# Performance work log

Hardware: AMD Instinct MI355X
Metric: run time of the kernel (lower is better)

Reference implementation:

```python
import jax, jax.numpy as jnp
import numpy as np

C = 1024
T = 2048
B = 8

def setup_inputs() -> dict:
    key = jax.random.key(0)
    ks = jax.random.split(key, 7)
    s = lambda fan_in: 1.0 / np.sqrt(fan_in)
    return {
        "x":     jax.random.normal(ks[0], (B, T, C), dtype=jnp.float32),
        "w_qkv": jax.random.uniform(ks[1], (C, 3 * C), jnp.float32, -s(C), s(C)),
        "w_proj": jax.random.uniform(ks[2], (C, C), jnp.float32, -s(C), s(C)),
        "w1":    jax.random.uniform(ks[3], (C, 2 * C), jnp.float32, -s(C), s(C)),
        "w2":    jax.random.uniform(ks[4], (2 * C, C), jnp.float32, -s(2 * C), s(2 * C)),
        "g1":    jnp.ones((C,), jnp.float32),
        "g2":    jnp.ones((C,), jnp.float32),
    }

def rmsnorm(x, g, eps=1e-6):
    return x * jax.lax.rsqrt(jnp.mean(x * x, axis=-1, keepdims=True) + eps) * g

def reference(x, w_qkv, w_proj, w1, w2, g1, g2):
    t = x.shape[1]
    # --- attention ---
    h = rmsnorm(x, g1)
    qkv = h @ w_qkv                               # [B,T,3C]
    q, k, v = jnp.split(qkv, 3, axis=-1)
    scores = jnp.einsum('bqc,bkc->bqk', q, k) * (C ** -0.5)  # [B,T,T]
    causal = jnp.triu(jnp.ones((t, t), dtype=bool), k=1)
    scores = jnp.where(causal, -jnp.inf, scores)
    attn = jax.nn.softmax(scores, axis=-1)
    x = x + (attn @ v) @ w_proj
    # --- ffn ---
    h = rmsnorm(x, g2)
    return x + (jax.nn.silu(h @ w1)) @ w2
```

## Files before the change

### kernel.cpp

```cpp
#include <hip/hip_runtime.h>
#include <hip/hip_bf16.h>
#include <stdint.h>


#define C_DIM 1024
#define T_DIM 2048
#define B_DIM 8

typedef float f32x4 __attribute__((ext_vector_type(4)));
typedef __bf16 bf16x8 __attribute__((ext_vector_type(8)));

typedef const __attribute__((address_space(1))) void gvoid_t;
typedef __attribute__((address_space(3))) void lvoid_t;

__device__ __forceinline__ void gload_lds16(const void* g, void* l) {
    __builtin_amdgcn_global_load_lds((gvoid_t*)g, (lvoid_t*)l, 16, 0, 0);
}

__device__ __forceinline__ unsigned short f2bf_bits(float f) {
    __hip_bfloat16 h = __float2bfloat16(f);
    return *reinterpret_cast<unsigned short*>(&h);
}

__device__ __forceinline__ void xcd_remap(int& bx, int& by, int& bz) {
    const int gx = gridDim.x, gy = gridDim.y;
    const int nwg = gx * gy * (int)gridDim.z;
    const int orig = bx + gx * (by + gy * bz);
    const int q = nwg >> 3, r = nwg & 7;
    const int xcd = orig & 7, pos = orig >> 3;
    const int neu = (xcd < r ? xcd * (q + 1) : r * (q + 1) + (xcd - r) * q) + pos;
    bx = neu % gx;
    const int t = neu / gx;
    by = t % gy;
    bz = t / gy;
}

#define RD_A(dst, buf, hq) do { \
    _Pragma("unroll") \
    for (int mf_ = 0; mf_ < 4; ++mf_) { \
        const char* p_ = lds + (buf)*32768 + wrb + (hq)*8192 + mf_*2048; \
        dst[mf_][0] = *(const bf16x8*)(p_ + offk0); \
        dst[mf_][1] = *(const bf16x8*)(p_ + offk1); \
    } \
} while(0)

#define RD_B(dst, buf, nh) do { \
    _Pragma("unroll") \
    for (int n2_ = 0; n2_ < 2; ++n2_) { \
        const char* p_ = lds + 65536 + (buf)*32768 + wcb + ((nh)*2 + n2_)*2048; \
        dst[n2_][0] = *(const bf16x8*)(p_ + offk0); \
        dst[n2_][1] = *(const bf16x8*)(p_ + offk1); \
    } \
} while(0)

#define MMQ(aS, bS, Mh, Nh) do { \
    _Pragma("unroll") \
    for (int m4_ = 0; m4_ < 4; ++m4_) \
    _Pragma("unroll") \
    for (int n2_ = 0; n2_ < 2; ++n2_) \
    _Pragma("unroll") \
    for (int ks_ = 0; ks_ < 2; ++ks_) \
        acc[(Mh)*4 + m4_][(Nh)*2 + n2_] = __builtin_amdgcn_mfma_f32_16x16x32_bf16( \
            aS[m4_][ks_], bS[n2_][ks_], acc[(Mh)*4 + m4_][(Nh)*2 + n2_], 0, 0, 0); \
} while(0)

#define STA(buf, half, kt) do { \
    const int go_ = aoff + (half)*128*lda + (kt)*64; \
    char* lp_ = ldsw + (buf)*32768 + (half)*16384; \
    gload_lds16(A + go_,            lp_); \
    gload_lds16(A + go_ + 64*lda,   lp_ + 8192); \
} while(0)
#define STB(buf, half, kt) do { \
    const int go_ = boff + (half)*128*ldb + (kt)*64; \
    char* lp_ = ldsw + 65536 + (buf)*32768 + (half)*16384; \
    gload_lds16(Bt + go_,           lp_); \
    gload_lds16(Bt + go_ + 64*ldb,  lp_ + 8192); \
} while(0)

#define TILE_BODY(t, STG) do { \
    const int buf_ = (t) & 1; \
    bf16x8 a0[4][2], a1[4][2], b0v[2][2], b1v[2][2]; \
    RD_A(a0, buf_, 0); RD_A(a1, buf_, 1); \
    RD_B(b0v, buf_, 0); RD_B(b1v, buf_, 1); \
    __builtin_amdgcn_s_setprio(1); \
    MMQ(a0, b0v, 0, 0); MMQ(a0, b1v, 0, 1); \
    MMQ(a1, b0v, 1, 0); MMQ(a1, b1v, 1, 1); \
    __builtin_amdgcn_s_setprio(0); \
    asm volatile("s_waitcnt lgkmcnt(0)" ::: "memory"); \
    asm volatile("s_waitcnt vmcnt(0)" ::: "memory"); \
    __builtin_amdgcn_s_barrier(); \
    if (STG) { STB(buf_,0,(t)+2); STB(buf_,1,(t)+2); \
               STA(buf_,0,(t)+2); STA(buf_,1,(t)+2); } \
} while(0)

template<int EPI, int CMODE>
__global__ __launch_bounds__(512, 2)
void gemm256(const __hip_bfloat16* A, const __hip_bfloat16* Bt,
             void* Cout, const float* R, void* C2, void* C3,
             int K, int lda, int ldb, int ldc,
             long long sA, long long sB, long long sC, float scale)
{
    int bx = blockIdx.x, by = blockIdx.y, bz = blockIdx.z;
    xcd_remap(bx, by, bz);
    if constexpr (CMODE == 1) { if (bx > by) return; }

    const int tid  = threadIdx.x;
    const int lane = tid & 63, wave = tid >> 6;
    const int l15  = lane & 15, l4 = lane >> 4;
    const int wr   = wave >> 2, wc = wave & 3;
    const int m0   = by * 256, n0 = bx * 256;
    const int z    = bz;

    A  += (long long)z * sA;
    Bt += (long long)z * sB;

    __shared__ __align__(16) char lds_[131072];
    char* lds  = lds_;
    char* ldsw = lds_ + wave * 1024;

    int kmax = K;
    if constexpr (CMODE == 2) { int km = m0 + 256; kmax = km < K ? km : K; }
    const int NT = kmax >> 6;

    const int offk0 = l15 * 128 + (((l4)     ^ (l15 & 7)) << 4);
    const int offk1 = l15 * 128 + (((4 + l4) ^ (l15 & 7)) << 4);
    const int wrb = wr * 16384, wcb = wc * 8192;

    const int rowq  = tid >> 3;
    const int sslot = (tid & 7) ^ (rowq & 7);
    const int aoff  = (m0 + rowq) * lda + sslot * 8;
    const int boff  = (n0 + rowq) * ldb + sslot * 8;

    f32x4 acc[8][4];
#pragma unroll
    for (int i = 0; i < 8; ++i)
#pragma unroll
        for (int j = 0; j < 4; ++j) acc[i][j] = (f32x4){0.f, 0.f, 0.f, 0.f};

    STB(0, 0, 0); STB(0, 1, 0); STA(0, 0, 0); STA(0, 1, 0);
    STB(1, 0, 1); STB(1, 1, 1); STA(1, 0, 1); STA(1, 1, 1);
    asm volatile("s_waitcnt vmcnt(8)" ::: "memory");
    __builtin_amdgcn_s_barrier();

    int t = 0;
    for (; t < NT - 2; ++t) TILE_BODY(t, true);
    for (; t < NT; ++t)     TILE_BODY(t, false);

    asm volatile("s_waitcnt vmcnt(0)" ::: "memory");

    const long long cbase = (long long)z * sC;
#pragma unroll
    for (int mf = 0; mf < 8; ++mf) {
        const int rbase = m0 + wr * 128 + mf * 16 + l4 * 4;
#pragma unroll
        for (int nf = 0; nf < 4; ++nf) {
            const int col = n0 + wc * 64 + nf * 16 + l15;
#pragma unroll
            for (int r = 0; r < 4; ++r) {
                const float v = acc[mf][nf][r];
                const int row = rbase + r;
                if constexpr (EPI == 6) {
                    const int seg = col >> 10, ncol = col & 1023;
                    if (seg == 0) {
                        ((__hip_bfloat16*)Cout)[(long long)row * 1024 + ncol] =
                            __float2bfloat16(v);
                    } else if (seg == 1) {
                        ((__hip_bfloat16*)C2)[(long long)row * 1024 + ncol] =
                            __float2bfloat16(v);
                    } else {
                        const int b = row >> 11, tt = row & 2047;
                        ((__hip_bfloat16*)C3)[((long long)b * C_DIM + ncol) * T_DIM + tt] =
                            __float2bfloat16(v);
                    }
                } else {
                    const long long idx = cbase + (long long)row * ldc + col;
                    if constexpr (EPI == 0) {
                        ((__hip_bfloat16*)Cout)[idx] = __float2bfloat16(v);
                    } else if constexpr (EPI == 2) {
                        ((float*)Cout)[idx] = v + R[idx];
                    } else if constexpr (EPI == 3) {
                        const float s = v / (1.f + __expf(-v));
                        ((__hip_bfloat16*)Cout)[idx] = __float2bfloat16(s);
                    } else {
                        ((__hip_bfloat16*)Cout)[idx] = __float2bfloat16(v * scale);
                    }
                }
            }
        }
    }
}

__global__ __launch_bounds__(256)
void rmsnorm_kernel(const float* __restrict__ x, const float* __restrict__ g,
                    __hip_bfloat16* __restrict__ out)
{
    const long long row = blockIdx.x;
    const int tid = threadIdx.x;
    const float4 v = ((const float4*)(x + row * C_DIM))[tid];
    float ss = v.x * v.x + v.y * v.y + v.z * v.z + v.w * v.w;
#pragma unroll
    for (int off = 32; off; off >>= 1) ss += __shfl_xor(ss, off);
    __shared__ float red[4];
    if ((tid & 63) == 0) red[tid >> 6] = ss;
    __syncthreads();
    ss = red[0] + red[1] + red[2] + red[3];
    const float sc = rsqrtf(ss * (1.0f / C_DIM) + 1e-6f);
    const float4 gv = ((const float4*)g)[tid];
    ushort4 u;
    u.x = f2bf_bits(v.x * sc * gv.x);
    u.y = f2bf_bits(v.y * sc * gv.y);
    u.z = f2bf_bits(v.z * sc * gv.z);
    u.w = f2bf_bits(v.w * sc * gv.w);
    *(ushort4*)(out + row * C_DIM + tid * 4) = u;
}

__global__ __launch_bounds__(256)
void softmax_causal(__hip_bfloat16* __restrict__ SP)
{
    const int i = blockIdx.x, b = blockIdx.y;
    __hip_bfloat16* row = SP + ((long long)b * T_DIM + i) * T_DIM;
    const int tid = threadIdx.x;
    const int jbase = tid * 8;

    uint4 raw = ((const uint4*)row)[tid];
    float v[8];
    const unsigned w[4] = {raw.x, raw.y, raw.z, raw.w};
#pragma unroll
    for (int c = 0; c < 4; ++c) {
        unsigned lo = w[c] << 16;
        unsigned hi = w[c] & 0xFFFF0000u;
        v[2 * c]     = __uint_as_float(lo);
        v[2 * c + 1] = __uint_as_float(hi);
    }
#pragma unroll
    for (int e = 0; e < 8; ++e)
        if (jbase + e > i) v[e] = -1e30f;

    float m = v[0];
#pragma unroll
    for (int e = 1; e < 8; ++e) m = fmaxf(m, v[e]);
#pragma unroll
    for (int off = 32; off; off >>= 1) m = fmaxf(m, __shfl_xor(m, off));
    __shared__ float redm[4], reds[4];
    if ((tid & 63) == 0) redm[tid >> 6] = m;
    __syncthreads();
    m = fmaxf(fmaxf(redm[0], redm[1]), fmaxf(redm[2], redm[3]));

    float e8[8];
    float s = 0.f;
#pragma unroll
    for (int e = 0; e < 8; ++e) { e8[e] = __expf(v[e] - m); s += e8[e]; }
#pragma unroll
    for (int off = 32; off; off >>= 1) s += __shfl_xor(s, off);
    if ((tid & 63) == 0) reds[tid >> 6] = s;
    __syncthreads();
    s = reds[0] + reds[1] + reds[2] + reds[3];
    const float inv = 1.f / s;

    uint4 outw;
    unsigned o[4];
#pragma unroll
    for (int c = 0; c < 4; ++c) {
        unsigned lo = f2bf_bits(e8[2 * c] * inv);
        unsigned hi = f2bf_bits(e8[2 * c + 1] * inv);
        o[c] = lo | (hi << 16);
    }
    outw.x = o[0]; outw.y = o[1]; outw.z = o[2]; outw.w = o[3];
    ((uint4*)row)[tid] = outw;
}

__global__ __launch_bounds__(256)
void wcast_t(const float* __restrict__ in, __hip_bfloat16* __restrict__ out,
             int K, int N)
{
    __shared__ float t[32][33];
    const int n0 = blockIdx.x * 32, k0 = blockIdx.y * 32;
    const int tx = threadIdx.x, ty = threadIdx.y;
#pragma unroll
    for (int r = ty; r < 32; r += 8)
        t[r][tx] = in[(long long)(k0 + r) * N + n0 + tx];
    __syncthreads();
#pragma unroll
    for (int r = ty; r < 32; r += 8)
        out[(long long)(n0 + r) * K + k0 + tx] = __float2bfloat16(t[tx][r]);
}

extern "C" void kernel_launch(void* const* d_in, const int* in_sizes, int n_in,
                              void* d_out, int out_size, void* d_ws, size_t ws_size,
                              hipStream_t stream)
{
    const float* x      = (const float*)d_in[0];
    const float* w_qkv  = (const float*)d_in[1];
    const float* w_proj = (const float*)d_in[2];
    const float* w1     = (const float*)d_in[3];
    const float* w2     = (const float*)d_in[4];
    const float* g1     = (const float*)d_in[5];
    const float* g2     = (const float*)d_in[6];
    float* out = (float*)d_out;
    char* ws = (char*)d_ws;

    const size_t SP_off = 0;
    const size_t h_off  = 0;
    const size_t u_off  = 0;
    const size_t q_off  = 67108864ull;
    const size_t k_off  = 100663296ull;
    const size_t vT_off = 134217728ull;
    const size_t wq_off = 167772160ull;
    const size_t wp_off = wq_off + 6291456ull;
    const size_t w1_off = wp_off + 2097152ull;
    const size_t w2_off = w1_off + 4194304ull;
    const size_t NEED   = w2_off + 4194304ull;

    if (ws_size < NEED) return;

    auto bf = [&](size_t off) { return (__hip_bfloat16*)(ws + off); };

    wcast_t<<<dim3(96, 32), dim3(32, 8), 0, stream>>>(w_qkv,  bf(wq_off), 1024, 3072);
    wcast_t<<<dim3(32, 32), dim3(32, 8), 0, stream>>>(w_proj, bf(wp_off), 1024, 1024);
    wcast_t<<<dim3(64, 32), dim3(32, 8), 0, stream>>>(w1,     bf(w1_off), 1024, 2048);
    wcast_t<<<dim3(32, 64), dim3(32, 8), 0, stream>>>(w2,     bf(w2_off), 2048, 1024);

    rmsnorm_kernel<<<16384, 256, 0, stream>>>(x, g1, bf(h_off));

    gemm256<6, 0><<<dim3(12, 64, 1), 512, 0, stream>>>(
        bf(h_off), bf(wq_off), bf(q_off), nullptr, bf(k_off), bf(vT_off),
        1024, 1024, 1024, 1024, 0, 0, 0, 1.f);

    gemm256<4, 1><<<dim3(8, 8, 8), 512, 0, stream>>>(
        bf(q_off), bf(k_off), bf(SP_off), nullptr, nullptr, nullptr,
        1024, 1024, 1024, 2048,
        (long long)T_DIM * C_DIM, (long long)T_DIM * C_DIM, (long long)T_DIM * T_DIM,
        0.03125f);

    softmax_causal<<<dim3(2048, 8), 256, 0, stream>>>(bf(SP_off));

    gemm256<0, 2><<<dim3(4, 8, 8), 512, 0, stream>>>(
        bf(SP_off), bf(vT_off), bf(k_off) , nullptr, nullptr, nullptr,
        2048, 2048, 2048, 1024,
        (long long)T_DIM * T_DIM, (long long)C_DIM * T_DIM, (long long)T_DIM * C_DIM,
        1.f);

    gemm256<2, 0><<<dim3(4, 64, 1), 512, 0, stream>>>(
        bf(k_off) , bf(wp_off), out, x, nullptr, nullptr,
        1024, 1024, 1024, 1024, 0, 0, 0, 1.f);

    rmsnorm_kernel<<<16384, 256, 0, stream>>>(out, g2, bf(q_off));

    gemm256<3, 0><<<dim3(8, 64, 1), 512, 0, stream>>>(
        bf(q_off), bf(w1_off), bf(u_off), nullptr, nullptr, nullptr,
        1024, 1024, 1024, 2048, 0, 0, 0, 1.f);

    gemm256<2, 0><<<dim3(4, 64, 1), 512, 0, stream>>>(
        bf(u_off), bf(w2_off), out, (const float*)out, nullptr, nullptr,
        2048, 2048, 2048, 1024, 0, 0, 0, 1.f);
}
```

Measured before the change: 583.5 us.

## Split QKV GEMM into three launches and use 128-tile kernels for attention

Replaces the fused QKV GEMM with three separate launches: a new 32x32x16 MFMA variant for Q, the 256 kernel for K, and a transposed-store epilogue for V. The batched attention score and PV GEMMs move to a new 128x128-tile kernel with 256 threads, a simple double-buffered K=32 loop and causal tile skipping. The aim is finer-grained causal work and better occupancy for the attention matmuls. The cost is extra launches and a less aggressively pipelined inner loop in the new 128-tile kernel.

```diff
diff --git a/kernel.cpp b/kernel.cpp
--- a/kernel.cpp
+++ b/kernel.cpp
@@ -7,7 +7,8 @@
 #define T_DIM 2048
 #define B_DIM 8
 
-typedef float f32x4 __attribute__((ext_vector_type(4)));
+typedef float f32x4  __attribute__((ext_vector_type(4)));
+typedef float f32x16 __attribute__((ext_vector_type(16)));
 typedef __bf16 bf16x8 __attribute__((ext_vector_type(8)));
 
 typedef const __attribute__((address_space(1))) void gvoid_t;
@@ -93,34 +94,26 @@
                STA(buf_,0,(t)+2); STA(buf_,1,(t)+2); } \
 } while(0)
 
-template<int EPI, int CMODE>
+template<int EPI>
 __global__ __launch_bounds__(512, 2)
 void gemm256(const __hip_bfloat16* A, const __hip_bfloat16* Bt,
-             void* Cout, const float* R, void* C2, void* C3,
-             int K, int lda, int ldb, int ldc,
-             long long sA, long long sB, long long sC, float scale)
+             void* Cout, const float* R,
+             int K, int lda, int ldb, int ldc)
 {
     int bx = blockIdx.x, by = blockIdx.y, bz = blockIdx.z;
     xcd_remap(bx, by, bz);
-    if constexpr (CMODE == 1) { if (bx > by) return; }
 
     const int tid  = threadIdx.x;
     const int lane = tid & 63, wave = tid >> 6;
     const int l15  = lane & 15, l4 = lane >> 4;
     const int wr   = wave >> 2, wc = wave & 3;
     const int m0   = by * 256, n0 = bx * 256;
-    const int z    = bz;
-
-    A  += (long long)z * sA;
-    Bt += (long long)z * sB;
 
     __shared__ __align__(16) char lds_[131072];
     char* lds  = lds_;
     char* ldsw = lds_ + wave * 1024;
 
-    int kmax = K;
-    if constexpr (CMODE == 2) { int km = m0 + 256; kmax = km < K ? km : K; }
-    const int NT = kmax >> 6;
+    const int NT = K >> 6;
 
     const int offk0 = l15 * 128 + (((l4)     ^ (l15 & 7)) << 4);
     const int offk1 = l15 * 128 + (((4 + l4) ^ (l15 & 7)) << 4);
@@ -148,7 +141,6 @@
 
     asm volatile("s_waitcnt vmcnt(0)" ::: "memory");
 
-    const long long cbase = (long long)z * sC;
 #pragma unroll
     for (int mf = 0; mf < 8; ++mf) {
         const int rbase = m0 + wr * 128 + mf * 16 + l4 * 4;
@@ -159,31 +151,215 @@
             for (int r = 0; r < 4; ++r) {
                 const float v = acc[mf][nf][r];
                 const int row = rbase + r;
-                if constexpr (EPI == 6) {
-                    const int seg = col >> 10, ncol = col & 1023;
-                    if (seg == 0) {
-                        ((__hip_bfloat16*)Cout)[(long long)row * 1024 + ncol] =
-                            __float2bfloat16(v);
-                    } else if (seg == 1) {
-                        ((__hip_bfloat16*)C2)[(long long)row * 1024 + ncol] =
-                            __float2bfloat16(v);
-                    } else {
-                        const int b = row >> 11, tt = row & 2047;
-                        ((__hip_bfloat16*)C3)[((long long)b * C_DIM + ncol) * T_DIM + tt] =
-                            __float2bfloat16(v);
-                    }
+                if constexpr (EPI == 5) {
+                    ((__hip_bfloat16*)Cout)[((long long)(row >> 11) * C_DIM + col) * T_DIM
+                                            + (row & 2047)] = __float2bfloat16(v);
                 } else {
-                    const long long idx = cbase + (long long)row * ldc + col;
+                    const long long idx = (long long)row * ldc + col;
                     if constexpr (EPI == 0) {
                         ((__hip_bfloat16*)Cout)[idx] = __float2bfloat16(v);
                     } else if constexpr (EPI == 2) {
                         ((float*)Cout)[idx] = v + R[idx];
-                    } else if constexpr (EPI == 3) {
+                    } else {
                         const float s = v / (1.f + __expf(-v));
                         ((__hip_bfloat16*)Cout)[idx] = __float2bfloat16(s);
-                    } else {
-                        ((__hip_bfloat16*)Cout)[idx] = __float2bfloat16(v * scale);
                     }
+                }
+            }
+        }
+    }
+}
+
+__global__ __launch_bounds__(512, 2)
+void gemm256_w32(const __hip_bfloat16* A, const __hip_bfloat16* Bt,
+                 void* Cout, int K, int lda, int ldb, int ldc)
+{
+    int bx = blockIdx.x, by = blockIdx.y, bz = blockIdx.z;
+    xcd_remap(bx, by, bz);
+
+    const int tid  = threadIdx.x;
+    const int lane = tid & 63, wave = tid >> 6;
+    const int l31  = lane & 31, l5 = lane >> 5;
+    const int wr   = wave >> 2, wc = wave & 3;
+    const int m0   = by * 256, n0 = bx * 256;
+
+    __shared__ __align__(16) char lds_[131072];
+    char* lds  = lds_;
+    char* ldsw = lds_ + wave * 1024;
+
+    const int NT = K >> 6;
+
+    const int rowq  = tid >> 3;
+    const int sslot = (tid & 7) ^ (rowq & 7);
+    const int aoff  = (m0 + rowq) * lda + sslot * 8;
+    const int boff  = (n0 + rowq) * ldb + sslot * 8;
+
+    f32x16 acc[4][2];
+#pragma unroll
+    for (int i = 0; i < 4; ++i)
+#pragma unroll
+        for (int j = 0; j < 2; ++j)
+#pragma unroll
+            for (int e = 0; e < 16; ++e) acc[i][j][e] = 0.f;
+
+    const int arowl = l31 & 7;
+
+    STB(0, 0, 0); STB(0, 1, 0); STA(0, 0, 0); STA(0, 1, 0);
+    STB(1, 0, 1); STB(1, 1, 1); STA(1, 0, 1); STA(1, 1, 1);
+    asm volatile("s_waitcnt vmcnt(8)" ::: "memory");
+    __builtin_amdgcn_s_barrier();
+
+    for (int t = 0; t < NT; ++t) {
+        const int buf_ = t & 1;
+        bf16x8 aR[4][4], bR[2][4];
+#pragma unroll
+        for (int mf = 0; mf < 4; ++mf) {
+            const int arow = wr * 128 + mf * 32 + l31;
+            const char* p_ = lds + buf_ * 32768 + arow * 128;
+#pragma unroll
+            for (int ks = 0; ks < 4; ++ks)
+                aR[mf][ks] = *(const bf16x8*)(p_ + ((((ks << 1) | l5) ^ arowl) << 4));
+        }
+#pragma unroll
+        for (int nf = 0; nf < 2; ++nf) {
+            const int bcol = wc * 64 + nf * 32 + l31;
+            const char* p_ = lds + 65536 + buf_ * 32768 + bcol * 128;
+#pragma unroll
+            for (int ks = 0; ks < 4; ++ks)
+                bR[nf][ks] = *(const bf16x8*)(p_ + ((((ks << 1) | l5) ^ arowl) << 4));
+        }
+        __builtin_amdgcn_s_setprio(1);
+#pragma unroll
+        for (int mf = 0; mf < 4; ++mf)
+#pragma unroll
+            for (int nf = 0; nf < 2; ++nf)
+#pragma unroll
+                for (int ks = 0; ks < 4; ++ks)
+                    acc[mf][nf] = __builtin_amdgcn_mfma_f32_32x32x16_bf16(
+                        aR[mf][ks], bR[nf][ks], acc[mf][nf], 0, 0, 0);
+        __builtin_amdgcn_s_setprio(0);
+        asm volatile("s_waitcnt lgkmcnt(0)" ::: "memory");
+        asm volatile("s_waitcnt vmcnt(0)" ::: "memory");
+        __builtin_amdgcn_s_barrier();
+        if (t + 2 < NT) {
+            STB(buf_, 0, t + 2); STB(buf_, 1, t + 2);
+            STA(buf_, 0, t + 2); STA(buf_, 1, t + 2);
+        }
+    }
+    asm volatile("s_waitcnt vmcnt(0)" ::: "memory");
+
+#pragma unroll
+    for (int mf = 0; mf < 4; ++mf)
+#pragma unroll
+        for (int nf = 0; nf < 2; ++nf) {
+            const int col = n0 + wc * 64 + nf * 32 + l31;
+#pragma unroll
+            for (int reg = 0; reg < 16; ++reg) {
+                const int row = m0 + wr * 128 + mf * 32
+                              + (reg & 3) + 8 * (reg >> 2) + 4 * l5;
+                ((__hip_bfloat16*)Cout)[(long long)row * ldc + col] =
+                    __float2bfloat16(acc[mf][nf][reg]);
+            }
+        }
+}
+
+template<int EPI, int CMODE>
+__global__ __launch_bounds__(256)
+void gemm128(const __hip_bfloat16* A, const __hip_bfloat16* Bt,
+             void* Cout, int K, int lda, int ldb, int ldc,
+             long long sA, long long sB, long long sC, float scale)
+{
+    int bx = blockIdx.x, by = blockIdx.y, bz = blockIdx.z;
+    xcd_remap(bx, by, bz);
+    if constexpr (CMODE == 1) { if (bx > by) return; }
+
+    const int tid  = threadIdx.x;
+    const int lane = tid & 63, wave = tid >> 6;
+    const int l15  = lane & 15, l4 = lane >> 4;
+    const int wr   = wave >> 1, wc = wave & 1;
+    const int m0   = by * 128, n0 = bx * 128;
+    const int z    = bz;
+
+    A  += (long long)z * sA;
+    Bt += (long long)z * sB;
+
+    __shared__ __align__(16) short As[2][128 * 32];
+    __shared__ __align__(16) short Bs[2][128 * 32];
+
+    int kmax = K;
+    if constexpr (CMODE == 2) { int km = m0 + 128; kmax = km < K ? km : K; }
+
+    f32x4 acc[4][4];
+#pragma unroll
+    for (int i = 0; i < 4; ++i)
+#pragma unroll
+        for (int j = 0; j < 4; ++j) acc[i][j] = (f32x4){0.f, 0.f, 0.f, 0.f};
+
+    const int srow  = wave * 32 + (lane >> 2);
+    const int sbyte = (((lane & 3) ^ ((lane >> 2) & 3))) << 4;
+    const char* Ag = (const char*)(A  + (long long)(m0 + srow) * lda) + sbyte;
+    const char* Bg = (const char*)(Bt + (long long)(n0 + srow) * ldb) + sbyte;
+    const long long astep = (long long)16 * lda * 2;
+    const long long bstep = (long long)16 * ldb * 2;
+    char* AsW[2] = {(char*)As[0] + wave * 2048, (char*)As[1] + wave * 2048};
+    char* BsW[2] = {(char*)Bs[0] + wave * 2048, (char*)Bs[1] + wave * 2048};
+
+    auto stage = [&](int buf, int k0) {
+        const char* ag = Ag + (long long)k0 * 2;
+        const char* bg = Bg + (long long)k0 * 2;
+        gload_lds16(ag,         AsW[buf]);
+        gload_lds16(ag + astep, AsW[buf] + 1024);
+        gload_lds16(bg,         BsW[buf]);
+        gload_lds16(bg + bstep, BsW[buf] + 1024);
+    };
+
+    const int cs16 = ((l4 ^ (l15 & 3)) << 4);
+
+    stage(0, 0);
+    __syncthreads();
+
+    for (int k0 = 0; k0 < kmax; k0 += 32) {
+        const int buf = (k0 >> 5) & 1;
+        if (k0 + 32 < kmax) stage(buf ^ 1, k0 + 32);
+
+        const char* Ac = (const char*)As[buf];
+        const char* Bc = (const char*)Bs[buf];
+        bf16x8 af[4], bfr[4];
+#pragma unroll
+        for (int mi = 0; mi < 4; ++mi) {
+            int row = wr * 64 + mi * 16 + l15;
+            af[mi] = *(const bf16x8*)(Ac + row * 64 + cs16);
+        }
+#pragma unroll
+        for (int ni = 0; ni < 4; ++ni) {
+            int col = wc * 64 + ni * 16 + l15;
+            bfr[ni] = *(const bf16x8*)(Bc + col * 64 + cs16);
+        }
+#pragma unroll
+        for (int mi = 0; mi < 4; ++mi)
+#pragma unroll
+            for (int ni = 0; ni < 4; ++ni)
+                acc[mi][ni] = __builtin_amdgcn_mfma_f32_16x16x32_bf16(
+                    af[mi], bfr[ni], acc[mi][ni], 0, 0, 0);
+
+        __syncthreads();
+    }
+
+    const long long cbase = (long long)z * sC;
+#pragma unroll
+    for (int mi = 0; mi < 4; ++mi) {
+        const int rbase = m0 + wr * 64 + mi * 16 + l4 * 4;
+#pragma unroll
+        for (int ni = 0; ni < 4; ++ni) {
+            const int col = n0 + wc * 64 + ni * 16 + l15;
+#pragma unroll
+            for (int r = 0; r < 4; ++r) {
+                const long long idx = cbase + (long long)(rbase + r) * ldc + col;
+                const float v = acc[mi][ni][r];
+                if constexpr (EPI == 0) {
+                    ((__hip_bfloat16*)Cout)[idx] = __float2bfloat16(v);
+                } else {
+                    ((__hip_bfloat16*)Cout)[idx] = __float2bfloat16(v * scale);
                 }
             }
         }
@@ -322,35 +498,40 @@
 
     rmsnorm_kernel<<<16384, 256, 0, stream>>>(x, g1, bf(h_off));
 
-    gemm256<6, 0><<<dim3(12, 64, 1), 512, 0, stream>>>(
-        bf(h_off), bf(wq_off), bf(q_off), nullptr, bf(k_off), bf(vT_off),
-        1024, 1024, 1024, 1024, 0, 0, 0, 1.f);
-
-    gemm256<4, 1><<<dim3(8, 8, 8), 512, 0, stream>>>(
-        bf(q_off), bf(k_off), bf(SP_off), nullptr, nullptr, nullptr,
+    gemm256_w32<<<dim3(4, 64, 1), 512, 0, stream>>>(
+        bf(h_off), bf(wq_off), bf(q_off), 1024, 1024, 1024, 1024);
+    gemm256<0><<<dim3(4, 64, 1), 512, 0, stream>>>(
+        bf(h_off), bf(wq_off) + 1024 * 1024, bf(k_off), nullptr,
+        1024, 1024, 1024, 1024);
+    gemm256<5><<<dim3(4, 64, 1), 512, 0, stream>>>(
+        bf(h_off), bf(wq_off) + 2 * 1024 * 1024, bf(vT_off), nullptr,
+        1024, 1024, 1024, 2048);
+
+    gemm128<4, 1><<<dim3(16, 16, 8), 256, 0, stream>>>(
+        bf(q_off), bf(k_off), bf(SP_off),
         1024, 1024, 1024, 2048,
         (long long)T_DIM * C_DIM, (long long)T_DIM * C_DIM, (long long)T_DIM * T_DIM,
         0.03125f);
 
     softmax_causal<<<dim3(2048, 8), 256, 0, stream>>>(bf(SP_off));
 
-    gemm256<0, 2><<<dim3(4, 8, 8), 512, 0, stream>>>(
-        bf(SP_off), bf(vT_off), bf(k_off) , nullptr, nullptr, nullptr,
+    gemm128<0, 2><<<dim3(8, 16, 8), 256, 0, stream>>>(
+        bf(SP_off), bf(vT_off), bf(k_off) ,
         2048, 2048, 2048, 1024,
         (long long)T_DIM * T_DIM, (long long)C_DIM * T_DIM, (long long)T_DIM * C_DIM,
         1.f);
 
-    gemm256<2, 0><<<dim3(4, 64, 1), 512, 0, stream>>>(
-        bf(k_off) , bf(wp_off), out, x, nullptr, nullptr,
-        1024, 1024, 1024, 1024, 0, 0, 0, 1.f);
+    gemm256<2><<<dim3(4, 64, 1), 512, 0, stream>>>(
+        bf(k_off) , bf(wp_off), out, x,
+        1024, 1024, 1024, 1024);
 
     rmsnorm_kernel<<<16384, 256, 0, stream>>>(out, g2, bf(q_off));
 
-    gemm256<3, 0><<<dim3(8, 64, 1), 512, 0, stream>>>(
-        bf(q_off), bf(w1_off), bf(u_off), nullptr, nullptr, nullptr,
-        1024, 1024, 1024, 2048, 0, 0, 0, 1.f);
-
-    gemm256<2, 0><<<dim3(4, 64, 1), 512, 0, stream>>>(
-        bf(u_off), bf(w2_off), out, (const float*)out, nullptr, nullptr,
-        2048, 2048, 2048, 1024, 0, 0, 0, 1.f);
-}
+    gemm256<3><<<dim3(8, 64, 1), 512, 0, stream>>>(
+        bf(q_off), bf(w1_off), bf(u_off), nullptr,
+        1024, 1024, 1024, 2048);
+
+    gemm256<2><<<dim3(4, 64, 1), 512, 0, stream>>>(
+        bf(u_off), bf(w2_off), out, (const float*)out,
+        2048, 2048, 2048, 1024);
+}
```

Result: faster. 549.3 us (-5.9%).
